# Performance work log

Measured on AMD Instinct MI355X. Metric: run time of the kernel, lower is better.

Reference implementation:

```python
import jax, jax.numpy as jnp
import numpy as np

B, N, F = 2, 2048, 256
H = 8
O = F // H  # nhid = 32
L = 3       # stacked GraphAttentionLayers
ALPHA = 0.2
NEG = jnp.float32(-1e15)


def setup_inputs() -> dict:
    key = jax.random.key(0)
    ks = jax.random.split(key, 6)
    x = jax.random.normal(ks[0], (B, N, F), dtype=jnp.float32)
    adj = jax.random.randint(ks[1], (B, N, N), 0, 2, dtype=jnp.int32)
    # per-layer multi-head params: W [L,H,F,O], a [L,H,2O]
    W_heads = jax.random.normal(ks[2], (L, H, F, O), dtype=jnp.float32) * 0.1
    a_heads = jax.random.normal(ks[3], (L, H, 2 * O), dtype=jnp.float32) * 0.1
    # per-layer out_att params (single head, F->F)
    W_out = jax.random.normal(ks[4], (L, F, F), dtype=jnp.float32) * 0.05
    a_out = jax.random.normal(ks[5], (L, 2 * F), dtype=jnp.float32) * 0.05
    return {"x": x, "adj": adj, "W_heads": W_heads, "a_heads": a_heads,
            "W_out": W_out, "a_out": a_out}


def _gat_heads(h, mask, W, a1, a2):
    """h: [B,N,F], mask: [B,N,N] bool, W: [H,F,O], a1/a2: [H,O] -> [B,H,N,O]."""
    Wh = jnp.einsum('bnf,hfo->bhno', h, W)
    s1 = jnp.einsum('bhno,ho->bhn', Wh, a1)   # a[:O] projection
    s2 = jnp.einsum('bhno,ho->bhn', Wh, a2)   # a[O:] projection
    e = s1[:, :, :, None] + s2[:, :, None, :]  # additive score [B,H,N,N]
    e = jnp.where(e > 0, e, ALPHA * e)         # LeakyReLU(alpha)
    e = jnp.where(mask[:, None, :, :], e, NEG)
    att = jax.nn.softmax(e, axis=-1)           # dropout is identity in eval
    hp = jnp.einsum('bhnm,bhmo->bhno', att, Wh)
    return jax.nn.elu(hp)                      # activate_function inside head


def reference(x, adj, W_heads, a_heads, W_out, a_out):
    mask = adj > 0
    h = x
    for l in range(L):
        a1 = a_heads[l, :, :O]
        a2 = a_heads[l, :, O:]
        hh = _gat_heads(h, mask, W_heads[l], a1, a2)      # [B,H,N,O]
        h = jnp.transpose(hh, (0, 2, 1, 3)).reshape(B, N, F)  # concat heads
        ao1 = a_out[l, :F][None]
        ao2 = a_out[l, F:][None]
        ho = _gat_heads(h, mask, W_out[l][None], ao1, ao2)[:, 0]  # [B,N,F]
        h = jax.nn.elu(ho)  # extra F.elu in GraphAttentionLayer (elu twice)
    return h
```

## Files before the change

### kernel.cpp

```cpp
#include <hip/hip_runtime.h>
#include <math.h>

#if __has_builtin(__builtin_amdgcn_exp2f)
#define EXP2(x) __builtin_amdgcn_exp2f(x)
#else
#define EXP2(x) exp2f(x)
#endif

#define ALPHA_LRELU 0.2f
#define LOG2E 1.4426950408889634f
#define ESHIFT 6.0f
#define BIGM 1024.0f

constexpr int Bc = 2, Nn = 2048, Ff = 256, Hh = 8, Oo = 32;

typedef _Float16 f16;
typedef f16 f16x8 __attribute__((ext_vector_type(8)));
typedef f16 f16x4 __attribute__((ext_vector_type(4)));
typedef float f32x4 __attribute__((ext_vector_type(4)));
typedef unsigned long long u64;
typedef unsigned u32;

__global__ __launch_bounds__(256) void zero_kernel(float* __restrict__ p) {
    p[blockIdx.x * 256 + threadIdx.x] = 0.f;
}

__global__ __launch_bounds__(256) void pack_kernel(
    const int* __restrict__ adj, u64* __restrict__ mask) {
    int idx = blockIdx.x * 256 + threadIdx.x;
    u64 b = __ballot(adj[idx] != 0);
    if ((threadIdx.x & 63) == 0) mask[idx >> 6] = b;
}

__global__ __launch_bounds__(256) void masktr_kernel(
    const u32* __restrict__ mw, u32* __restrict__ mt) {
    int idx = blockIdx.x * 256 + threadIdx.x;
    int i = idx & 2047;
    int c = (idx >> 11) & 63;
    int b = idx >> 17;
    mt[idx] = mw[((size_t)b * 2048 + i) * 64 + c];
}

__global__ __launch_bounds__(256) void wt_kernel(
    const float* __restrict__ W_heads, const float* __restrict__ W_out,
    f16* __restrict__ WTF) {
    int t = threadIdx.x;
    int y = blockIdx.y;
    int l = y >> 1, st = y & 1;
    int col = blockIdx.x * 4 + (t >> 6);
    int k0 = (t & 63) * 4;
    const float* src;
    int stride;
    if (st == 0) {
        src = W_heads + (((size_t)l * Hh + (col >> 5)) * Ff) * Oo + (col & 31);
        stride = Oo;
    } else {
        src = W_out + (size_t)l * Ff * Ff + col;
        stride = Ff;
    }
    f16x4 v;
#pragma unroll
    for (int i = 0; i < 4; ++i) v[i] = (f16)src[(size_t)(k0 + i) * stride];
    int cg = col >> 4, am = col & 15;
    int c = k0 >> 5, aq = (k0 >> 3) & 3, i0 = k0 & 7;
    WTF += (((size_t)y * 16 + cg) * 8 + c) * 512 + (aq * 16 + am) * 8 + i0;
    *(f16x4*)WTF = v;
}

__global__ __launch_bounds__(256) void apack_kernel(
    const float* __restrict__ A, f16* __restrict__ Af) {
    int t = threadIdx.x;
    int lane = t & 63;
    int slot = blockIdx.x * 4 + (t >> 6);
    int am = lane & 15, aq = lane >> 4;
    int mt = slot >> 3, c = slot & 7;
    const float* ap = A + ((size_t)mt * 16 + am) * Ff + c * 32 + aq * 8;
    f32x4 v0 = *(const f32x4*)ap;
    f32x4 v1 = *(const f32x4*)(ap + 4);
    f16x8 o;
#pragma unroll
    for (int i = 0; i < 4; ++i) { o[i] = (f16)v0[i]; o[4 + i] = (f16)v1[i]; }
    *(f16x8*)&Af[(size_t)slot * 512 + lane * 8] = o;
}

__global__ __launch_bounds__(256) void gemm_wave(
    const f16* __restrict__ Af, const f16* __restrict__ WTF,
    const float* __restrict__ pa, f16* __restrict__ WhFrag,
    float* __restrict__ s1, float* __restrict__ s2,
    int G, int Ofull, int oshift) {
    int t = threadIdx.x;
    int w = t >> 6, lane = t & 63;
    int am = lane & 15, aq = lane >> 4;
    int mt = blockIdx.x * 4 + w;
    int colb = blockIdx.y * 16;

    const f16* ap = Af + (size_t)(mt * 8) * 512 + lane * 8;
    const f16* bp = WTF + (size_t)((colb >> 4) * 8) * 512 + lane * 8;

    f32x4 acc = {0.f, 0.f, 0.f, 0.f};
    f16x8 a0 = *(const f16x8*)ap;
    f16x8 b0 = *(const f16x8*)bp;
#pragma unroll
    for (int c = 0; c < 8; ++c) {
        int cn = (c + 1 < 8) ? c + 1 : 0;
        f16x8 an = *(const f16x8*)(ap + cn * 512);
        f16x8 bn = *(const f16x8*)(bp + cn * 512);
        acc = __builtin_amdgcn_mfma_f32_16x16x32_f16(a0, b0, acc, 0, 0, 0);
        a0 = an; b0 = bn;
    }

    int m0 = mt * 16;
    int b = m0 >> 11;
    int nn0 = (m0 & 2047) + aq * 4;
    int cO = (m0 & 2047) >> 5;
    int aq_p = ((mt & 1) << 1) | (aq >> 1);
    int i0p = (aq & 1) << 2;
    int g = colb >> oshift;
    size_t bg = (size_t)b * G + g;
    int cg = (colb & (Ofull - 1)) >> 4;

    f16x4 c4;
#pragma unroll
    for (int e = 0; e < 4; ++e) c4[e] = (f16)acc[e];
    *(f16x4*)&WhFrag[(((bg * (Ofull >> 4) + cg) * 64 + cO) * 512) +
                     (aq_p * 16 + am) * 8 + i0p] = c4;

    int o0 = (colb & (Ofull - 1)) + am;
    const float* a1p = pa + 2 * (size_t)g * Ofull;
    float a10 = a1p[o0];
    float a20 = a1p[Ofull + o0];
#pragma unroll
    for (int e = 0; e < 4; ++e) {
        float p1 = acc[e] * a10;
        float p2 = acc[e] * a20;
#pragma unroll
        for (int s = 1; s < 16; s <<= 1) {
            p1 += __shfl_xor(p1, s);
            p2 += __shfl_xor(p2, s);
        }
        if (am == 0) {
            size_t sidx = bg * Nn + nn0 + e;
            atomicAdd(&s1[sidx], p1);
            atomicAdd(&s2[sidx], p2);
        }
    }
}

template <bool OUT, bool FINAL>
__global__ __launch_bounds__(256) void attn_kernel(
    const f16* __restrict__ WhFrag, const float* __restrict__ s1,
    const float* __restrict__ s2, const u32* __restrict__ maskT,
    float* __restrict__ dst, f16* __restrict__ AfOut) {
    constexpr float C0 = -ESHIFT * LOG2E - BIGM;
    constexpr int NCG = OUT ? 16 : 2;
    constexpr int TSTR = 40;
    __shared__ f16 T[4][16 * TSTR];

    int t = threadIdx.x;
    int w = t >> 6, lane = t & 63;
    int am = lane & 15, aq = lane >> 4;
    int i0 = blockIdx.x * 64 + w * 16;
    int bz = blockIdx.z;
    int b = OUT ? bz : (bz >> 3);
    int cg0 = OUT ? blockIdx.y * 2 : 0;
    int dstcol = OUT ? cg0 * 16 : (bz & 7) * Oo;

    const f16* bp0 = WhFrag + ((size_t)bz * NCG + cg0) * 64 * 512 + lane * 8;
    const f16* bp1 = bp0 + 64 * 512;
    const float* s2p = s2 + (size_t)bz * Nn + aq * 8;
    float s1v = s1[(size_t)bz * Nn + i0 + am];
    const u32* mtp = maskT + (size_t)b * 64 * 2048 + i0 + am;

    f32x4 acc0 = {0.f, 0.f, 0.f, 0.f}, acc1 = acc0;
    float lacc = 0.f;

    f16x8 xb0 = *(const f16x8*)bp0;
    f16x8 xb1 = *(const f16x8*)bp1;
    f32x4 xv0 = *(const f32x4*)s2p;
    f32x4 xv1 = *(const f32x4*)(s2p + 4);
    u32 xm = mtp[0];

    for (int c = 0; c < 64; ++c) {
        int cn = (c + 1 < 64) ? c + 1 : 0;
        f16x8 nb0 = *(const f16x8*)(bp0 + cn * 512);
        f16x8 nb1 = *(const f16x8*)(bp1 + cn * 512);
        f32x4 nv0 = *(const f32x4*)(s2p + cn * 32);
        f32x4 nv1 = *(const f32x4*)(s2p + cn * 32 + 4);
        u32 nm = mtp[cn * 2048];

        u32 bits = (xm >> (aq * 8)) & 0xffu;
        f16x8 af;
#pragma unroll
        for (int k = 0; k < 8; ++k) {
            float xv = s1v + (k < 4 ? xv0[k] : xv1[k - 4]);
            float lr = fmaxf(xv, ALPHA_LRELU * xv);
            float bitf = (float)((bits >> k) & 1u);
            float p = EXP2(fmaf(bitf, BIGM, fmaf(lr, LOG2E, C0)));
            lacc += p;
            af[k] = (f16)p;
        }
        acc0 = __builtin_amdgcn_mfma_f32_16x16x32_f16(af, xb0, acc0, 0, 0, 0);
        acc1 = __builtin_amdgcn_mfma_f32_16x16x32_f16(af, xb1, acc1, 0, 0, 0);
        xb0 = nb0; xb1 = nb1; xv0 = nv0; xv1 = nv1; xm = nm;
    }

    lacc += __shfl_xor(lacc, 16);
    lacc += __shfl_xor(lacc, 32);

    f16* Tw = T[w];
#pragma unroll
    for (int e = 0; e < 4; ++e) {
        int r = aq * 4 + e;
        float li = __shfl(lacc, r);
        float v0 = acc0[e] / li, v1 = acc1[e] / li;
        v0 = v0 > 0.f ? v0 : __expf(v0) - 1.f;
        v1 = v1 > 0.f ? v1 : __expf(v1) - 1.f;
        if (OUT) {
            v0 = v0 > 0.f ? v0 : __expf(v0) - 1.f;
            v1 = v1 > 0.f ? v1 : __expf(v1) - 1.f;
        }
        if (FINAL) {
            size_t base = ((size_t)b * Nn + i0 + r) * Ff + dstcol;
            dst[base + am] = v0;
            dst[base + 16 + am] = v1;
        } else {
            Tw[r * TSTR + am] = (f16)v0;
            Tw[r * TSTR + 16 + am] = (f16)v1;
        }
    }
    if (!FINAL) {
        f16x8 o = *(const f16x8*)&Tw[am * TSTR + aq * 8];
        int mt = (b * Nn + i0) >> 4;
        int c = dstcol >> 5;
        *(f16x8*)&AfOut[(size_t)(mt * 8 + c) * 512 + lane * 8] = o;
    }
}

extern "C" void kernel_launch(void* const* d_in, const int* in_sizes, int n_in,
                              void* d_out, int out_size, void* d_ws, size_t ws_size,
                              hipStream_t stream) {
    const float* x = (const float*)d_in[0];
    const int* adj = (const int*)d_in[1];
    const float* W_heads = (const float*)d_in[2];
    const float* a_heads = (const float*)d_in[3];
    const float* W_out = (const float*)d_in[4];
    const float* a_out = (const float*)d_in[5];
    float* out = (float*)d_out;

    float* ws = (float*)d_ws;
    const size_t M = (size_t)Bc * Nn * Ff;
    f16* Af_a = (f16*)ws;
    f16* Af_b = (f16*)(ws + M / 2);
    f16* WhFrag = (f16*)(ws + M);
    u64* maskW = (u64*)(ws + 3 * M / 2);
    u32* maskT = (u32*)(ws + 3 * M / 2 + M / 4);
    f16* WTF = (f16*)(ws + 3 * M / 2 + M / 2);
    float* sbuf = ws + 3 * M / 2 + M / 2 + 196608;
    const size_t SH = (size_t)Bc * Hh * Nn;
    const size_t SO = (size_t)Bc * Nn;
    const size_t SL = 2 * SH + 2 * SO;

    zero_kernel<<<(3 * SL) / 256, 256, 0, stream>>>(sbuf);
    pack_kernel<<<(Bc * Nn * Nn) / 256, 256, 0, stream>>>(adj, maskW);
    masktr_kernel<<<(Bc * 64 * 2048) / 256, 256, 0, stream>>>((const u32*)maskW, maskT);
    wt_kernel<<<dim3(Ff / 4, 6), 256, 0, stream>>>(W_heads, W_out, WTF);
    apack_kernel<<<(Bc * Nn * Ff / 8) / 256, 256, 0, stream>>>(x, Af_a);

    for (int l = 0; l < 3; ++l) {
        float* s1h = sbuf + l * SL;
        float* s2h = s1h + SH;
        float* s1o = s2h + SH;
        float* s2o = s1o + SO;

        gemm_wave<<<dim3((Bc * Nn) / 64, Ff / 16), 256, 0, stream>>>(
            Af_a, WTF + (size_t)(2 * l) * Ff * Ff,
            a_heads + (size_t)l * Hh * 2 * Oo, WhFrag, s1h, s2h, Hh, Oo, 5);
        attn_kernel<false, false><<<dim3(Nn / 64, 1, Bc * Hh), 256, 0, stream>>>(
            WhFrag, s1h, s2h, maskT, nullptr, Af_b);

        gemm_wave<<<dim3((Bc * Nn) / 64, Ff / 16), 256, 0, stream>>>(
            Af_b, WTF + (size_t)(2 * l + 1) * Ff * Ff,
            a_out + (size_t)l * 2 * Ff, WhFrag, s1o, s2o, 1, Ff, 8);
        if (l == 2) {
            attn_kernel<true, true><<<dim3(Nn / 64, Ff / 32, Bc), 256, 0, stream>>>(
                WhFrag, s1o, s2o, maskT, out, nullptr);
        } else {
            attn_kernel<true, false><<<dim3(Nn / 64, Ff / 32, Bc), 256, 0, stream>>>(
                WhFrag, s1o, s2o, maskT, nullptr, Af_a);
        }
    }
}
```

Measured before the change: 309.2 us.

## Split attention key loop across wave pairs and fuse mask pack with transpose

Each attention block now covers 32 rows instead of 64. Two waves split the 64 key chunks for each 16-row tile, and their partial accumulators and row sums are combined through shared memory. The main loop is unrolled by two with double-buffered prefetch. Separately, the adjacency ballot writes the transposed 32-bit mask words directly, which removes the masktr kernel and its intermediate buffer. This doubles the block count for better occupancy and latency hiding, at the cost of an extra __syncthreads, shared-memory reduction traffic, and idle waves during the epilogue.

```diff
diff --git a/kernel.cpp b/kernel.cpp
--- a/kernel.cpp
+++ b/kernel.cpp
@@ -26,19 +26,18 @@
 }
 
 __global__ __launch_bounds__(256) void pack_kernel(
-    const int* __restrict__ adj, u64* __restrict__ mask) {
+    const int* __restrict__ adj, u32* __restrict__ maskT) {
     int idx = blockIdx.x * 256 + threadIdx.x;
-    u64 b = __ballot(adj[idx] != 0);
-    if ((threadIdx.x & 63) == 0) mask[idx >> 6] = b;
-}
-
-__global__ __launch_bounds__(256) void masktr_kernel(
-    const u32* __restrict__ mw, u32* __restrict__ mt) {
-    int idx = blockIdx.x * 256 + threadIdx.x;
-    int i = idx & 2047;
-    int c = (idx >> 11) & 63;
-    int b = idx >> 17;
-    mt[idx] = mw[((size_t)b * 2048 + i) * 64 + c];
+    u64 bl = __ballot(adj[idx] != 0);
+    int lane = threadIdx.x & 63;
+    int i = (idx >> 11) & 2047;
+    int b = idx >> 22;
+    int j0 = (idx & 2047) & ~63;
+    int c32 = j0 >> 5;
+    if (lane == 0)
+        maskT[((size_t)b * 64 + c32) * 2048 + i] = (u32)bl;
+    else if (lane == 1)
+        maskT[((size_t)b * 64 + c32 + 1) * 2048 + i] = (u32)(bl >> 32);
 }
 
 __global__ __launch_bounds__(256) void wt_kernel(
@@ -154,12 +153,16 @@
     constexpr float C0 = -ESHIFT * LOG2E - BIGM;
     constexpr int NCG = OUT ? 16 : 2;
     constexpr int TSTR = 40;
-    __shared__ f16 T[4][16 * TSTR];
+    __shared__ float Ls[4][64];
+    __shared__ float As[4][64][8];
+    __shared__ f16 T[2][16 * TSTR];
 
     int t = threadIdx.x;
     int w = t >> 6, lane = t & 63;
     int am = lane & 15, aq = lane >> 4;
-    int i0 = blockIdx.x * 64 + w * 16;
+    int wr = w & 1;
+    int wh = w >> 1;
+    int i0 = blockIdx.x * 32 + wr * 16;
     int bz = blockIdx.z;
     int b = OUT ? bz : (bz >> 3);
     int cg0 = OUT ? blockIdx.y * 2 : 0;
@@ -174,65 +177,89 @@
     f32x4 acc0 = {0.f, 0.f, 0.f, 0.f}, acc1 = acc0;
     float lacc = 0.f;
 
-    f16x8 xb0 = *(const f16x8*)bp0;
-    f16x8 xb1 = *(const f16x8*)bp1;
-    f32x4 xv0 = *(const f32x4*)s2p;
-    f32x4 xv1 = *(const f32x4*)(s2p + 4);
-    u32 xm = mtp[0];
-
-    for (int c = 0; c < 64; ++c) {
-        int cn = (c + 1 < 64) ? c + 1 : 0;
-        f16x8 nb0 = *(const f16x8*)(bp0 + cn * 512);
-        f16x8 nb1 = *(const f16x8*)(bp1 + cn * 512);
-        f32x4 nv0 = *(const f32x4*)(s2p + cn * 32);
-        f32x4 nv1 = *(const f32x4*)(s2p + cn * 32 + 4);
-        u32 nm = mtp[cn * 2048];
-
-        u32 bits = (xm >> (aq * 8)) & 0xffu;
+    int cbeg = wh * 32, cend = cbeg + 32;
+
+    f16x8 xb0, xb1, yb0, yb1;
+    f32x4 xv0, xv1, yv0, yv1;
+    u32 xm, ym;
+    auto ld = [&](int c, f16x8& b0, f16x8& b1, f32x4& v0, f32x4& v1, u32& m) {
+        b0 = *(const f16x8*)(bp0 + c * 512);
+        b1 = *(const f16x8*)(bp1 + c * 512);
+        v0 = *(const f32x4*)(s2p + c * 32);
+        v1 = *(const f32x4*)(s2p + c * 32 + 4);
+        m = mtp[c * 2048];
+    };
+    auto comp = [&](f16x8 b0, f16x8 b1, f32x4 v0, f32x4 v1, u32 m) {
+        u32 bits = (m >> (aq * 8)) & 0xffu;
         f16x8 af;
 #pragma unroll
         for (int k = 0; k < 8; ++k) {
-            float xv = s1v + (k < 4 ? xv0[k] : xv1[k - 4]);
+            float xv = s1v + (k < 4 ? v0[k] : v1[k - 4]);
             float lr = fmaxf(xv, ALPHA_LRELU * xv);
             float bitf = (float)((bits >> k) & 1u);
             float p = EXP2(fmaf(bitf, BIGM, fmaf(lr, LOG2E, C0)));
             lacc += p;
             af[k] = (f16)p;
         }
-        acc0 = __builtin_amdgcn_mfma_f32_16x16x32_f16(af, xb0, acc0, 0, 0, 0);
-        acc1 = __builtin_amdgcn_mfma_f32_16x16x32_f16(af, xb1, acc1, 0, 0, 0);
-        xb0 = nb0; xb1 = nb1; xv0 = nv0; xv1 = nv1; xm = nm;
+        acc0 = __builtin_amdgcn_mfma_f32_16x16x32_f16(af, b0, acc0, 0, 0, 0);
+        acc1 = __builtin_amdgcn_mfma_f32_16x16x32_f16(af, b1, acc1, 0, 0, 0);
+    };
+
+    ld(cbeg, xb0, xb1, xv0, xv1, xm);
+    ld(cbeg + 1, yb0, yb1, yv0, yv1, ym);
+    for (int c = cbeg; c < cend; c += 2) {
+        comp(xb0, xb1, xv0, xv1, xm);
+        ld(c + 2 < cend ? c + 2 : cbeg, xb0, xb1, xv0, xv1, xm);
+        comp(yb0, yb1, yv0, yv1, ym);
+        ld(c + 3 < cend ? c + 3 : cbeg, yb0, yb1, yv0, yv1, ym);
     }
 
     lacc += __shfl_xor(lacc, 16);
     lacc += __shfl_xor(lacc, 32);
 
-    f16* Tw = T[w];
+    Ls[w][lane] = lacc;
 #pragma unroll
     for (int e = 0; e < 4; ++e) {
-        int r = aq * 4 + e;
-        float li = __shfl(lacc, r);
-        float v0 = acc0[e] / li, v1 = acc1[e] / li;
-        v0 = v0 > 0.f ? v0 : __expf(v0) - 1.f;
-        v1 = v1 > 0.f ? v1 : __expf(v1) - 1.f;
-        if (OUT) {
+        As[w][lane][e] = acc0[e];
+        As[w][lane][4 + e] = acc1[e];
+    }
+    __syncthreads();
+
+    if (wh == 0) {
+        float lt = Ls[w][lane] + Ls[w + 2][lane];
+        f32x4 a0, a1;
+#pragma unroll
+        for (int e = 0; e < 4; ++e) {
+            a0[e] = As[w][lane][e] + As[w + 2][lane][e];
+            a1[e] = As[w][lane][4 + e] + As[w + 2][lane][4 + e];
+        }
+        f16* Tw = T[wr];
+#pragma unroll
+        for (int e = 0; e < 4; ++e) {
+            int r = aq * 4 + e;
+            float li = __shfl(lt, r);
+            float v0 = a0[e] / li, v1 = a1[e] / li;
             v0 = v0 > 0.f ? v0 : __expf(v0) - 1.f;
             v1 = v1 > 0.f ? v1 : __expf(v1) - 1.f;
-        }
-        if (FINAL) {
-            size_t base = ((size_t)b * Nn + i0 + r) * Ff + dstcol;
-            dst[base + am] = v0;
-            dst[base + 16 + am] = v1;
-        } else {
-            Tw[r * TSTR + am] = (f16)v0;
-            Tw[r * TSTR + 16 + am] = (f16)v1;
-        }
-    }
-    if (!FINAL) {
-        f16x8 o = *(const f16x8*)&Tw[am * TSTR + aq * 8];
-        int mt = (b * Nn + i0) >> 4;
-        int c = dstcol >> 5;
-        *(f16x8*)&AfOut[(size_t)(mt * 8 + c) * 512 + lane * 8] = o;
+            if (OUT) {
+                v0 = v0 > 0.f ? v0 : __expf(v0) - 1.f;
+                v1 = v1 > 0.f ? v1 : __expf(v1) - 1.f;
+            }
+            if (FINAL) {
+                size_t base = ((size_t)b * Nn + i0 + r) * Ff + dstcol;
+                dst[base + am] = v0;
+                dst[base + 16 + am] = v1;
+            } else {
+                Tw[r * TSTR + am] = (f16)v0;
+                Tw[r * TSTR + 16 + am] = (f16)v1;
+            }
+        }
+        if (!FINAL) {
+            f16x8 o = *(const f16x8*)&Tw[am * TSTR + aq * 8];
+            int mt = (b * Nn + i0) >> 4;
+            int c = dstcol >> 5;
+            *(f16x8*)&AfOut[(size_t)(mt * 8 + c) * 512 + lane * 8] = o;
+        }
     }
 }
 
@@ -252,17 +279,15 @@
     f16* Af_a = (f16*)ws;
     f16* Af_b = (f16*)(ws + M / 2);
     f16* WhFrag = (f16*)(ws + M);
-    u64* maskW = (u64*)(ws + 3 * M / 2);
-    u32* maskT = (u32*)(ws + 3 * M / 2 + M / 4);
-    f16* WTF = (f16*)(ws + 3 * M / 2 + M / 2);
-    float* sbuf = ws + 3 * M / 2 + M / 2 + 196608;
+    u32* maskT = (u32*)(ws + 3 * M / 2);
+    f16* WTF = (f16*)(ws + 3 * M / 2 + M / 4);
+    float* sbuf = ws + 3 * M / 2 + M / 4 + 196608;
     const size_t SH = (size_t)Bc * Hh * Nn;
     const size_t SO = (size_t)Bc * Nn;
     const size_t SL = 2 * SH + 2 * SO;
 
     zero_kernel<<<(3 * SL) / 256, 256, 0, stream>>>(sbuf);
-    pack_kernel<<<(Bc * Nn * Nn) / 256, 256, 0, stream>>>(adj, maskW);
-    masktr_kernel<<<(Bc * 64 * 2048) / 256, 256, 0, stream>>>((const u32*)maskW, maskT);
+    pack_kernel<<<(Bc * Nn * Nn) / 256, 256, 0, stream>>>(adj, maskT);
     wt_kernel<<<dim3(Ff / 4, 6), 256, 0, stream>>>(W_heads, W_out, WTF);
     apack_kernel<<<(Bc * Nn * Ff / 8) / 256, 256, 0, stream>>>(x, Af_a);
 
@@ -275,17 +300,17 @@
         gemm_wave<<<dim3((Bc * Nn) / 64, Ff / 16), 256, 0, stream>>>(
             Af_a, WTF + (size_t)(2 * l) * Ff * Ff,
             a_heads + (size_t)l * Hh * 2 * Oo, WhFrag, s1h, s2h, Hh, Oo, 5);
-        attn_kernel<false, false><<<dim3(Nn / 64, 1, Bc * Hh), 256, 0, stream>>>(
+        attn_kernel<false, false><<<dim3(Nn / 32, 1, Bc * Hh), 256, 0, stream>>>(
             WhFrag, s1h, s2h, maskT, nullptr, Af_b);
 
         gemm_wave<<<dim3((Bc * Nn) / 64, Ff / 16), 256, 0, stream>>>(
             Af_b, WTF + (size_t)(2 * l + 1) * Ff * Ff,
             a_out + (size_t)l * 2 * Ff, WhFrag, s1o, s2o, 1, Ff, 8);
         if (l == 2) {
-            attn_kernel<true, true><<<dim3(Nn / 64, Ff / 32, Bc), 256, 0, stream>>>(
+            attn_kernel<true, true><<<dim3(Nn / 32, Ff / 32, Bc), 256, 0, stream>>>(
                 WhFrag, s1o, s2o, maskT, out, nullptr);
         } else {
-            attn_kernel<true, false><<<dim3(Nn / 64, Ff / 32, Bc), 256, 0, stream>>>(
+            attn_kernel<true, false><<<dim3(Nn / 32, Ff / 32, Bc), 256, 0, stream>>>(
                 WhFrag, s1o, s2o, maskT, nullptr, Af_a);
         }
     }
```

After: 301.7 us. 1.02x faster.
